# Optimization experiments

Measured on AMD Instinct MI355X. Metric: run time of the kernel, lower is better.

Reference implementation:

```python
import jax, jax.numpy as jnp
import numpy as np

B, T, N = 16, 512, 128
D, HID, S, H, L, EMB = 256, 128, 16, 512, 4, 512
EPS_BN = 1e-5
EPS_LN = 1e-5


def _ln(x, w, b):
    mu = x.mean(-1, keepdims=True)
    v = ((x - mu) ** 2).mean(-1, keepdims=True)
    return (x - mu) * jax.lax.rsqrt(v + EPS_LN) * w + b


def _bn(x, w, b):
    # x: (M, N, C); training-mode BatchNorm1d over (batch, spatial), biased var
    mu = x.mean((0, 1))
    v = x.var((0, 1))
    return (x - mu) * jax.lax.rsqrt(v + EPS_BN) * w + b


def setup_inputs() -> dict:
    key = jax.random.key(0)
    ks = iter(jax.random.split(key, 40))
    r = lambda *s: jax.random.normal(next(ks), s, jnp.float32) * 0.05
    inp = dict(
        x=jax.random.normal(next(ks), (B, T, N, 3), jnp.float32),
        lengths=jax.random.randint(next(ks), (B,), 0, T),
        conv1_w=r(HID, 3), bn1_w=1.0 + r(HID), bn1_b=r(HID),
        conv2_w=r(HID, HID), bn2_w=1.0 + r(HID), bn2_b=r(HID),
        fproj_w=r(D, HID), fproj_b=r(D),
        pre_ln_w=1.0 + r(D), pre_ln_b=r(D),
        in_w=r(L, 2 * H, D), in_b=r(L, 2 * H),
        conv_w=r(L, H, 1, 4), conv_b=r(L, H),
        A=r(L, H, S), Bm=r(L, H, S),
        out_w=r(L, D, H), out_b=r(L, D),
        post_ln_w=1.0 + r(D), post_ln_b=r(D),
        m1_w=r(1024, D), m1_b=r(1024),
        m2_w=r(1024, 1024), m2_b=r(1024),
        m3_w=r(EMB, 1024), m3_b=r(EMB),
    )
    return inp


def reference(x, lengths, conv1_w, bn1_w, bn1_b, conv2_w, bn2_w, bn2_b,
              fproj_w, fproj_b, pre_ln_w, pre_ln_b,
              in_w, in_b, conv_w, conv_b, A, Bm, out_w, out_b,
              post_ln_w, post_ln_b, m1_w, m1_b, m2_w, m2_b, m3_w, m3_b):
    Bb, Tt, Nn, _ = x.shape
    xf = x.reshape(Bb * Tt, Nn, 3)
    mu = xf.mean(1, keepdims=True)
    sd = jnp.std(xf, axis=1, ddof=1, keepdims=True) + 1e-10  # torch.std unbiased
    xn = (xf - mu) / sd

    # PointNet frame encoder (1x1 convs == per-point matmuls)
    h1 = jax.nn.relu(_bn(xn @ conv1_w.T, bn1_w, bn1_b))      # (BT, N, HID)
    h2 = jax.nn.relu(_bn(h1 @ conv2_w.T, bn2_w, bn2_b))
    feat = h2.max(1) @ fproj_w.T + fproj_b                   # (BT, D)

    seq = _ln(feat.reshape(Bb, Tt, D), pre_ln_w, pre_ln_b)
    mask = (jnp.arange(Tt)[None, :] < lengths[:, None]).astype(seq.dtype)  # (B, T)
    mk = mask[:, :, None]

    def mamba(seq, iw, ib, cw, cb, Ai, Bi, ow, ob):
        inp = seq @ iw.T + ib                                # (B, T, 2H)
        Hh = inp.shape[-1] // 2
        gate = jax.nn.sigmoid(inp[..., :Hh])
        upd = jax.nn.silu(inp[..., Hh:])
        u = jax.lax.conv_general_dilated(
            upd.transpose(0, 2, 1), cw, (1,), [(2, 2)],
            feature_group_count=Hh, dimension_numbers=('NCH', 'OIH', 'NCH'))
        u = (u + cb[:, None])[:, :, :seq.shape[1]].transpose(0, 2, 1)  # drop extra step
        # masked linear state scan == masked cumulative sum
        Bu = jnp.einsum('bth,hs->bts', u, Bi) * mk           # (B, T, S)
        hstate = jnp.cumsum(Bu, axis=1)
        out = jnp.einsum('bts,hs->bth', hstate, Ai) * gate * mk
        return out @ ow.T + ob

    for i in range(L):
        seq = mamba(seq, in_w[i], in_b[i], conv_w[i], conv_b[i], A[i], Bm[i], out_w[i], out_b[i])

    seq = _ln(seq, post_ln_w, post_ln_b)
    denom = jnp.maximum(lengths, 1).astype(seq.dtype)[:, None]
    pooled = (seq * mk).sum(1) / denom

    e = jax.nn.gelu(pooled @ m1_w.T + m1_b, approximate=False)
    e = jax.nn.gelu(e @ m2_w.T + m2_b, approximate=False)
    e = e @ m3_w.T + m3_b
    return e / jnp.maximum(jnp.linalg.norm(e, axis=1, keepdims=True), 1e-12)
```

## Files before the change

kernel.cpp:

```cpp
#include <hip/hip_runtime.h>
#include <hip/hip_bf16.h>
#include <math.h>

#define NFRM 8192
#define NPT  128
#define CH   128
#define DD   256
#define HH   512
#define SS   16
#define NL   4

typedef __attribute__((ext_vector_type(8))) short bf16x8;
typedef __attribute__((ext_vector_type(4))) float f32x4;
typedef unsigned short u16;

#define MFMA16 __builtin_amdgcn_mfma_f32_16x16x32_bf16


__device__ __forceinline__ float red256(float v, int tid, volatile float* sc) {
#pragma unroll
  for (int off = 32; off; off >>= 1) v += __shfl_down(v, off);
  __syncthreads();
  if ((tid & 63) == 0) sc[tid >> 6] = v;
  __syncthreads();
  return sc[0] + sc[1] + sc[2] + sc[3];
}

__device__ __forceinline__ float sigmoidf_(float x) { return 1.f / (1.f + __expf(-x)); }
__device__ __forceinline__ float geluf_(float x) { return 0.5f * x * (1.f + erff(x * 0.70710678118654752f)); }

__device__ __forceinline__ u16 f2bf(float f) {
  __hip_bfloat16 h = __float2bfloat16(f);
  return *(u16*)&h;
}
__device__ __forceinline__ float bf2f(u16 u) {
  union { unsigned int i; float f; } v; v.i = ((unsigned int)u) << 16; return v.f;
}


__global__ __launch_bounds__(256) void k_prep(const float* __restrict__ conv2_w,
    const float* __restrict__ fproj_w, const float* __restrict__ in_w, const float* __restrict__ out_w,
    const float* __restrict__ A, const float* __restrict__ Bm,
    const float* __restrict__ cw, const float* __restrict__ cb,
    u16* __restrict__ W2B, u16* __restrict__ fprojB, u16* __restrict__ inwB,
    u16* __restrict__ outwB, u16* __restrict__ albB, u16* __restrict__ BmTd,
    float* __restrict__ cbB) {
  int idx = blockIdx.x * 256 + threadIdx.x;
  if (idx < 16384) {
    int c = idx >> 7, k = idx & 127;
    int dst = c * 128 + ((((k >> 3) ^ (c & 7)) << 3) | (k & 7));
    W2B[dst] = f2bf(conv2_w[idx]);
    return;
  }
  idx -= 16384;
  if (idx < 8192) {
    float4 v = ((const float4*)fproj_w)[idx];
    ushort4 o; o.x = f2bf(v.x); o.y = f2bf(v.y); o.z = f2bf(v.z); o.w = f2bf(v.w);
    ((ushort4*)fprojB)[idx] = o;
    return;
  }
  idx -= 8192;
  if (idx < 262144) {
    float4 v = ((const float4*)in_w)[idx];
    ushort4 o; o.x = f2bf(v.x); o.y = f2bf(v.y); o.z = f2bf(v.z); o.w = f2bf(v.w);
    ((ushort4*)inwB)[idx] = o;
    return;
  }
  idx -= 262144;
  if (idx < 131072) {
    float4 v = ((const float4*)out_w)[idx];
    ushort4 o; o.x = f2bf(v.x); o.y = f2bf(v.y); o.z = f2bf(v.z); o.w = f2bf(v.w);
    ((ushort4*)outwB)[idx] = o;
    return;
  }
  idx -= 131072;
  if (idx < 65536) {
    int l = idx >> 14, rem = idx & 16383, h = rem >> 5, kk = rem & 31;
    albB[idx] = (kk < 16) ? f2bf(A[(size_t)l * 8192 + h * 16 + kk]) : (u16)0;
    return;
  }
  idx -= 65536;
  if (idx < 131072) {
    int l = idx >> 15, rem = idx & 32767;
    int d = rem >> 13, rem2 = rem & 8191, s = rem2 >> 9, h = rem2 & 511;
    BmTd[idx] = f2bf(cw[(size_t)l * 2048 + h * 4 + d] * Bm[(size_t)l * 8192 + h * 16 + s]);
    return;
  }
  idx -= 131072;
  if (idx < 4096) {
    int wsl = idx >> 6, lane = idx & 63;
    int l = wsl >> 4, s = wsl & 15;
    float acc = 0.f;
    for (int h = lane; h < 512; h += 64)
      acc = fmaf(cb[l * 512 + h], Bm[(size_t)l * 8192 + h * 16 + s], acc);
#pragma unroll
    for (int off = 32; off; off >>= 1) acc += __shfl_down(acc, off);
    if (lane == 0) cbB[wsl] = acc;
  }
}

__global__ __launch_bounds__(256) void k_mom(const float* __restrict__ x, float* __restrict__ msd,
                                             float* __restrict__ pstat) {
  __shared__ float mpart[4][6];
  int tid = threadIdx.x, lane = tid & 63, w = tid >> 6;
  int f = blockIdx.x * 4 + w;
  const float* xf = x + (size_t)f * 384 + lane * 6;
  float a0 = xf[0], a1 = xf[1], a2 = xf[2], b0 = xf[3], b1 = xf[4], b2 = xf[5];
  float s0 = a0 + b0, s1 = a1 + b1, s2 = a2 + b2;
  float p00 = a0*a0 + b0*b0, p01 = a0*a1 + b0*b1, p02 = a0*a2 + b0*b2;
  float p11 = a1*a1 + b1*b1, p12 = a1*a2 + b1*b2, p22 = a2*a2 + b2*b2;
#pragma unroll
  for (int off = 32; off; off >>= 1) {
    s0 += __shfl_down(s0, off); s1 += __shfl_down(s1, off); s2 += __shfl_down(s2, off);
    p00 += __shfl_down(p00, off); p01 += __shfl_down(p01, off); p02 += __shfl_down(p02, off);
    p11 += __shfl_down(p11, off); p12 += __shfl_down(p12, off); p22 += __shfl_down(p22, off);
  }
  if (lane == 0) {
    float mu0 = s0 * (1.f/128.f), mu1 = s1 * (1.f/128.f), mu2 = s2 * (1.f/128.f);
    float C00 = p00 - 128.f*mu0*mu0, C01 = p01 - 128.f*mu0*mu1, C02 = p02 - 128.f*mu0*mu2;
    float C11 = p11 - 128.f*mu1*mu1, C12 = p12 - 128.f*mu1*mu2, C22 = p22 - 128.f*mu2*mu2;
    float sd0 = sqrtf(C00 * (1.f/127.f)) + 1e-10f;
    float sd1 = sqrtf(C11 * (1.f/127.f)) + 1e-10f;
    float sd2 = sqrtf(C22 * (1.f/127.f)) + 1e-10f;
    mpart[w][0] = C00/(sd0*sd0); mpart[w][1] = C01/(sd0*sd1); mpart[w][2] = C02/(sd0*sd2);
    mpart[w][3] = C11/(sd1*sd1); mpart[w][4] = C12/(sd1*sd2); mpart[w][5] = C22/(sd2*sd2);
    float* d = msd + (size_t)f * 8;
    d[0] = mu0; d[1] = mu1; d[2] = mu2; d[3] = 0.f;
    d[4] = 1.f/sd0; d[5] = 1.f/sd1; d[6] = 1.f/sd2; d[7] = 0.f;
  }
  __syncthreads();
  if (tid < 8) {
    float tot = 0.f;
    if (tid < 6) { for (int w2 = 0; w2 < 4; ++w2) tot += mpart[w2][tid]; }
    pstat[blockIdx.x * 8 + tid] = tot;
  }
}

__global__ __launch_bounds__(256) void k_stats2(const float* __restrict__ pstat, const float* __restrict__ w1,
    const float* __restrict__ bw, const float* __restrict__ bb, float* __restrict__ cc) {
  __shared__ float part[32][8];
  __shared__ float Mt[8];
  int tid = threadIdx.x, j = tid & 7, g = tid >> 3;
  float sm = 0.f;
  for (int r = g; r < 2048; r += 32) sm += pstat[r * 8 + j];
  part[g][j] = sm;
  __syncthreads();
  if (tid < 8) { float tot = 0.f; for (int g2 = 0; g2 < 32; ++g2) tot += part[g2][tid]; Mt[tid] = tot; }
  __syncthreads();
  if (tid < 128) {
    float w0 = w1[tid*3], wa = w1[tid*3+1], wb = w1[tid*3+2];
    float var = (w0*w0*Mt[0] + wa*wa*Mt[3] + wb*wb*Mt[5]
               + 2.f*(w0*wa*Mt[1] + w0*wb*Mt[2] + wa*wb*Mt[4])) * (1.f/1048576.f);
    float s = bw[tid] / sqrtf(var + 1e-5f);
    ((float4*)cc)[tid] = make_float4(s*w0, s*wa, s*wb, bb[tid]);
  }
}

__global__ __launch_bounds__(256) void k2_main(const float* __restrict__ x, const float4* __restrict__ cc,
    const float4* __restrict__ msd4, const u16* __restrict__ W2B,
    float* __restrict__ z2mx, float* __restrict__ z2mn,
    float* __restrict__ psum, float* __restrict__ psq) {
  __shared__ alignas(16) u16 w2s[16384];
  __shared__ float4 ccs[144];
  __shared__ float smx[2][4][CH], smn[2][4][CH], ssm[2][4][CH], ssq[2][4][CH];
  int tid = threadIdx.x;
  for (int i = tid; i < 2048; i += 256) ((float4*)w2s)[i] = ((const float4*)W2B)[i];
  if (tid < 128) ccs[tid + (tid >> 3)] = cc[tid];
  int lane = tid & 63, w = tid >> 6;
  int lr = lane & 15, kg = lane >> 4;
  int row0 = w * 32 + lr, row1 = row0 + 16;
  int f0i = blockIdx.x * 8;
  float4 mu4 = msd4[f0i * 2], rs4 = msd4[f0i * 2 + 1];
  const float* xr0 = x + (size_t)f0i * 384 + row0 * 3;
  const float* xr1 = x + (size_t)f0i * 384 + row1 * 3;
  float cx0 = xr0[0], cx1 = xr0[1], cx2 = xr0[2];
  float cx3 = xr1[0], cx4 = xr1[1], cx5 = xr1[2];
  __syncthreads();
  for (int fi = 0; fi < 8; ++fi) {
    int f = blockIdx.x * 8 + fi;
    int p = fi & 1;
    float xa0 = (cx0 - mu4.x) * rs4.x, xa1 = (cx1 - mu4.y) * rs4.y, xa2 = (cx2 - mu4.z) * rs4.z;
    float xb0 = (cx3 - mu4.x) * rs4.x, xb1 = (cx4 - mu4.y) * rs4.y, xb2 = (cx5 - mu4.z) * rs4.z;
    int fn = (f + 1 < NFRM) ? f + 1 : f;
    float4 nmu = msd4[fn * 2], nrs = msd4[fn * 2 + 1];
    const float* nr0 = x + (size_t)fn * 384 + row0 * 3;
    const float* nr1 = x + (size_t)fn * 384 + row1 * 3;
    float nx0 = nr0[0], nx1 = nr0[1], nx2 = nr0[2];
    float nx3 = nr1[0], nx4 = nr1[1], nx5 = nr1[2];
    f32x4 acc[2][8];
#pragma unroll
    for (int fr = 0; fr < 2; ++fr)
#pragma unroll
      for (int fc = 0; fc < 8; ++fc) acc[fr][fc] = (f32x4){0.f, 0.f, 0.f, 0.f};
#pragma unroll
    for (int ks = 0; ks < 4; ++ks) {
      int kc = ks * 4 + kg;
      int base9 = kc * 9;
      bf16x8 a0, a1;
#pragma unroll
      for (int q = 0; q < 8; ++q) {
        float4 c4 = ccs[base9 + q];
        float h0 = fmaxf(0.f, fmaf(xa0, c4.x, fmaf(xa1, c4.y, fmaf(xa2, c4.z, c4.w))));
        float h1 = fmaxf(0.f, fmaf(xb0, c4.x, fmaf(xb1, c4.y, fmaf(xb2, c4.z, c4.w))));
        a0[q] = (short)f2bf(h0); a1[q] = (short)f2bf(h1);
      }
#pragma unroll
      for (int fc = 0; fc < 8; ++fc) {
        int col = fc * 16 + lr;
        bf16x8 b = *(const bf16x8*)&w2s[col * 128 + ((kc ^ (col & 7)) << 3)];
        acc[0][fc] = MFMA16(a0, b, acc[0][fc], 0, 0, 0);
        acc[1][fc] = MFMA16(a1, b, acc[1][fc], 0, 0, 0);
      }
    }
#pragma unroll
    for (int fc = 0; fc < 8; ++fc) {
      float mx = -3e38f, mn = 3e38f, sm = 0.f, sq = 0.f;
#pragma unroll
      for (int fr = 0; fr < 2; ++fr)
#pragma unroll
        for (int r = 0; r < 4; ++r) {
          float v = acc[fr][fc][r];
          mx = fmaxf(mx, v); mn = fminf(mn, v); sm += v; sq = fmaf(v, v, sq);
        }
#pragma unroll
      for (int off = 16; off <= 32; off <<= 1) {
        mx = fmaxf(mx, __shfl_xor(mx, off));
        mn = fminf(mn, __shfl_xor(mn, off));
        sm += __shfl_xor(sm, off);
        sq += __shfl_xor(sq, off);
      }
      if (lane < 16) {
        int col = fc * 16 + lr;
        smx[p][w][col] = mx; smn[p][w][col] = mn; ssm[p][w][col] = sm; ssq[p][w][col] = sq;
      }
    }
    __syncthreads();
    if (tid < CH) {
      float mx = smx[p][0][tid], mn = smn[p][0][tid], sm = ssm[p][0][tid], sq = ssq[p][0][tid];
#pragma unroll
      for (int w2 = 1; w2 < 4; ++w2) {
        mx = fmaxf(mx, smx[p][w2][tid]); mn = fminf(mn, smn[p][w2][tid]);
        sm += ssm[p][w2][tid]; sq += ssq[p][w2][tid];
      }
      z2mx[(size_t)f * CH + tid] = mx;
      z2mn[(size_t)f * CH + tid] = mn;
      psum[(size_t)f * CH + tid] = sm;
      psq[(size_t)f * CH + tid]  = sq;
    }
    cx0 = nx0; cx1 = nx1; cx2 = nx2; cx3 = nx3; cx4 = nx4; cx5 = nx5;
    mu4 = nmu; rs4 = nrs;
  }
}

__global__ __launch_bounds__(256) void k_red1(const float* __restrict__ psum, const float* __restrict__ psq,
    float* __restrict__ prs, float* __restrict__ prq) {
  __shared__ float s0[2][128], s1[2][128];
  int tid = threadIdx.x, c = tid & 127, half = tid >> 7;
  int f0 = blockIdx.x * 128;
  float sm = 0.f, sq = 0.f;
  for (int fl = half; fl < 128; fl += 2) {
    size_t idx = (size_t)(f0 + fl) * 128 + c;
    sm += psum[idx]; sq += psq[idx];
  }
  s0[half][c] = sm; s1[half][c] = sq;
  __syncthreads();
  if (tid < 128) {
    prs[blockIdx.x * 128 + tid] = s0[0][tid] + s0[1][tid];
    prq[blockIdx.x * 128 + tid] = s1[0][tid] + s1[1][tid];
  }
}

__global__ __launch_bounds__(256) void k_red2(const float* __restrict__ prs, const float* __restrict__ prq,
    const float* __restrict__ w, const float* __restrict__ b, float* __restrict__ st,
    float invM, float eps) {
  __shared__ float s0[2][128], s1[2][128];
  int tid = threadIdx.x, c = tid & 127, half = tid >> 7;
  float sm = 0.f, sq = 0.f;
  for (int g = half; g < 64; g += 2) { sm += prs[g * 128 + c]; sq += prq[g * 128 + c]; }
  s0[half][c] = sm; s1[half][c] = sq;
  __syncthreads();
  if (tid < 128) {
    float tsm = s0[0][tid] + s0[1][tid], tsq = s1[0][tid] + s1[1][tid];
    float mean = tsm * invM;
    float var = tsq * invM - mean * mean;
    float s = w[tid] / sqrtf(var + eps);
    st[tid] = s;
    st[CH + tid] = b[tid] - mean * s;
  }
}

__global__ __launch_bounds__(512) void k_fi(const float* __restrict__ z2mx, const float* __restrict__ z2mn,
    const float* __restrict__ s2t2, const u16* __restrict__ fprojB, const float* __restrict__ fpb,
    const float* __restrict__ plw, const float* __restrict__ plb,
    const u16* __restrict__ inwB_l, const float* __restrict__ inb,
    u16* __restrict__ gate, u16* __restrict__ upd) {
  __shared__ alignas(16) u16 h2s[32 * 128];
  __shared__ float ft[32 * 260];
  __shared__ alignas(16) u16 as[32 * 256];
  int f0 = blockIdx.x * 32, tid = threadIdx.x;
  int lane = tid & 63, w = tid >> 6, lr = lane & 15, kg = lane >> 4;
  {
    int row = tid >> 4, cc = tid & 15, c0 = cc * 8;
    const float* zx = z2mx + (size_t)(f0 + row) * 128 + c0;
    const float* zn = z2mn + (size_t)(f0 + row) * 128 + c0;
    bf16x8 v;
#pragma unroll
    for (int q = 0; q < 8; ++q) {
      int c = c0 + q;
      float s = s2t2[c], t = s2t2[128 + c];
      float z = (s >= 0.f) ? zx[q] : zn[q];
      v[q] = (short)f2bf(fmaxf(0.f, fmaf(s, z, t)));
    }
    *(bf16x8*)&h2s[row * 128 + ((cc ^ (row & 7)) << 3)] = v;
  }
  __syncthreads();
  {
    f32x4 fac[2][2];
#pragma unroll
    for (int fr = 0; fr < 2; ++fr)
#pragma unroll
      for (int fc = 0; fc < 2; ++fc) fac[fr][fc] = (f32x4){0.f, 0.f, 0.f, 0.f};
#pragma unroll
    for (int ks = 0; ks < 4; ++ks) {
      int kc = ks * 4 + kg;
      bf16x8 a0 = *(const bf16x8*)&h2s[lr * 128 + ((kc ^ (lr & 7)) << 3)];
      bf16x8 a1 = *(const bf16x8*)&h2s[(16 + lr) * 128 + ((kc ^ (lr & 7)) << 3)];
#pragma unroll
      for (int fc = 0; fc < 2; ++fc) {
        int d = w * 32 + fc * 16 + lr;
        bf16x8 b = *(const bf16x8*)&fprojB[(size_t)d * 128 + kc * 8];
        fac[0][fc] = MFMA16(a0, b, fac[0][fc], 0, 0, 0);
        fac[1][fc] = MFMA16(a1, b, fac[1][fc], 0, 0, 0);
      }
    }
#pragma unroll
    for (int fr = 0; fr < 2; ++fr)
#pragma unroll
      for (int fc = 0; fc < 2; ++fc) {
        int d = w * 32 + fc * 16 + lr;
        float bias = fpb[d];
#pragma unroll
        for (int r = 0; r < 4; ++r) {
          int row = fr * 16 + kg * 4 + r;
          ft[row * 260 + d] = fac[fr][fc][r] + bias;
        }
      }
  }
  __syncthreads();
  {
    float4 plw4 = ((const float4*)plw)[lane];
    float4 plb4 = ((const float4*)plb)[lane];
#pragma unroll
    for (int q = 0; q < 4; ++q) {
      int row = w * 4 + q;
      float4 v = *(const float4*)&ft[row * 260 + lane * 4];
      float s = v.x + v.y + v.z + v.w;
#pragma unroll
      for (int off = 32; off; off >>= 1) s += __shfl_xor(s, off);
      float mu = s * (1.f / 256.f);
      float4 dd = make_float4(v.x - mu, v.y - mu, v.z - mu, v.w - mu);
      float qq = dd.x*dd.x + dd.y*dd.y + dd.z*dd.z + dd.w*dd.w;
#pragma unroll
      for (int off = 32; off; off >>= 1) qq += __shfl_xor(qq, off);
      float rs = 1.f / sqrtf(qq * (1.f / 256.f) + 1e-5f);
      u16 o[4];
      o[0] = f2bf(fmaf(dd.x * rs, plw4.x, plb4.x));
      o[1] = f2bf(fmaf(dd.y * rs, plw4.y, plb4.y));
      o[2] = f2bf(fmaf(dd.z * rs, plw4.z, plb4.z));
      o[3] = f2bf(fmaf(dd.w * rs, plw4.w, plb4.w));
      int chunk = lane >> 1;
      *(uint2*)&as[row * 256 + ((chunk ^ (row & 7)) << 3) + (lane & 1) * 4] = *(uint2*)o;
    }
  }
  __syncthreads();
  f32x4 acc[2][8];
#pragma unroll
  for (int fr = 0; fr < 2; ++fr)
#pragma unroll
    for (int fc = 0; fc < 8; ++fc) acc[fr][fc] = (f32x4){0.f, 0.f, 0.f, 0.f};
  int colb = w * 128;
#pragma unroll
  for (int ks = 0; ks < 8; ++ks) {
    int kc = ks * 4 + kg;
    int r1 = 16 + lr;
    bf16x8 a0 = *(const bf16x8*)&as[lr * 256 + ((kc ^ (lr & 7)) << 3)];
    bf16x8 a1 = *(const bf16x8*)&as[r1 * 256 + ((kc ^ (r1 & 7)) << 3)];
#pragma unroll
    for (int fc = 0; fc < 8; ++fc) {
      int col = colb + fc * 16 + lr;
      bf16x8 b = *(const bf16x8*)&inwB_l[(size_t)col * 256 + kc * 8];
      acc[0][fc] = MFMA16(a0, b, acc[0][fc], 0, 0, 0);
      acc[1][fc] = MFMA16(a1, b, acc[1][fc], 0, 0, 0);
    }
  }
  bool isGate = (w < 4);
  u16* dst = isGate ? gate : upd;
  int cbOff = isGate ? 0 : 512;
#pragma unroll
  for (int fr = 0; fr < 2; ++fr)
#pragma unroll
    for (int fc = 0; fc < 8; ++fc) {
      int cg = colb + fc * 16 + lr;
      float bias = inb[cg];
      int colOut = cg - cbOff;
#pragma unroll
      for (int r = 0; r < 4; ++r) {
        int frame = f0 + fr * 16 + kg * 4 + r;
        float v = acc[fr][fc][r] + bias;
        float sg = sigmoidf_(v);
        v = isGate ? sg : v * sg;
        dst[(size_t)frame * 512 + colOut] = f2bf(v);
      }
    }
}

__global__ __launch_bounds__(256) void k_bu(const u16* __restrict__ updB, const u16* __restrict__ BmTd_l,
    const float* __restrict__ cbB_l, const int* __restrict__ lengths, float* __restrict__ bu) {
  __shared__ float part[2][32][16];
  int tid = threadIdx.x, lane = tid & 63, w = tid >> 6;
  int wf = w & 1, hh = w >> 1;
  int f0 = blockIdx.x * 32 + wf * 16;
  int lr = lane & 15, kg = lane >> 4;
  int t = (f0 & 511) + lr;
  const u16* arow = updB + (size_t)(f0 + lr) * 512;
  bool v0 = (t >= 2), v1 = (t >= 1), v3 = (t <= 510);
  const bf16x8 zv = (bf16x8){0,0,0,0,0,0,0,0};
  f32x4 acc = (f32x4){0.f, 0.f, 0.f, 0.f};
#pragma unroll
  for (int ks = 0; ks < 8; ++ks) {
    int kc = hh * 32 + ks * 4 + kg, co = kc * 8;
    bf16x8 a0 = v0 ? *(const bf16x8*)&arow[co - 1024] : zv;
    bf16x8 a1 = v1 ? *(const bf16x8*)&arow[co - 512]  : zv;
    bf16x8 a2 =      *(const bf16x8*)&arow[co];
    bf16x8 a3 = v3 ? *(const bf16x8*)&arow[co + 512]  : zv;
    acc = MFMA16(a0, *(const bf16x8*)&BmTd_l[0 * 8192 + lr * 512 + co], acc, 0, 0, 0);
    acc = MFMA16(a1, *(const bf16x8*)&BmTd_l[1 * 8192 + lr * 512 + co], acc, 0, 0, 0);
    acc = MFMA16(a2, *(const bf16x8*)&BmTd_l[2 * 8192 + lr * 512 + co], acc, 0, 0, 0);
    acc = MFMA16(a3, *(const bf16x8*)&BmTd_l[3 * 8192 + lr * 512 + co], acc, 0, 0, 0);
  }
#pragma unroll
  for (int r = 0; r < 4; ++r) part[hh][wf * 16 + kg * 4 + r][lr] = acc[r];
  __syncthreads();
  int len = lengths[blockIdx.x >> 4];
  for (int i = tid; i < 512; i += 256) {
    int fl = i >> 4, s = i & 15;
    int frame = blockIdx.x * 32 + fl;
    int tt = frame & 511, bi = frame >> 9;
    float val = part[0][fl][s] + part[1][fl][s] + cbB_l[s];
    bu[((size_t)bi * 16 + s) * 512 + tt] = (tt < len) ? val : 0.f;
  }
}

__global__ __launch_bounds__(512) void k_mo(const float* __restrict__ bu,
    u16* __restrict__ gateB, u16* __restrict__ updB,
    const u16* __restrict__ albB_l, const u16* __restrict__ outwB_l, const float* __restrict__ outb,
    const u16* __restrict__ inwB_n, const float* __restrict__ inb_n,
    const int* __restrict__ lengths) {
  __shared__ alignas(16) u16 hsb[32 * 40];
  __shared__ alignas(16) u16 vl[32 * 512];
  __shared__ alignas(16) u16 as[32 * 256];
  int f0 = blockIdx.x * 32, tid = threadIdx.x;
  int bb = f0 >> 9, tbase = f0 & 511;
  int len = lengths[bb];
  int lane = tid & 63, w = tid >> 6, lr = lane & 15, kg = lane >> 4;
  for (int i = tid; i < 640; i += 512) ((unsigned int*)hsb)[i] = 0;
  __syncthreads();
#pragma unroll
  for (int q = 0; q < 2; ++q) {
    int s = w * 2 + q;
    const float* src = bu + ((size_t)bb * 16 + s) * 512 + lane * 8;
    float4 v0 = *(const float4*)src, v1 = *(const float4*)(src + 4);
    float p0 = v0.x, p1 = p0 + v0.y, p2 = p1 + v0.z, p3 = p2 + v0.w;
    float p4 = p3 + v1.x, p5 = p4 + v1.y, p6 = p5 + v1.z, p7 = p6 + v1.w;
    float tot = p7;
#pragma unroll
    for (int off = 1; off < 64; off <<= 1) {
      float n = __shfl_up(tot, off);
      if (lane >= off) tot += n;
    }
    float excl = tot - p7;
    int rbase = lane * 8 - tbase;
    if (rbase >= 0 && rbase < 32) {
      hsb[(rbase + 0) * 40 + s] = f2bf(p0 + excl);
      hsb[(rbase + 1) * 40 + s] = f2bf(p1 + excl);
      hsb[(rbase + 2) * 40 + s] = f2bf(p2 + excl);
      hsb[(rbase + 3) * 40 + s] = f2bf(p3 + excl);
      hsb[(rbase + 4) * 40 + s] = f2bf(p4 + excl);
      hsb[(rbase + 5) * 40 + s] = f2bf(p5 + excl);
      hsb[(rbase + 6) * 40 + s] = f2bf(p6 + excl);
      hsb[(rbase + 7) * 40 + s] = f2bf(p7 + excl);
    }
  }
  __syncthreads();
  {
    bf16x8 a0 = *(const bf16x8*)&hsb[lr * 40 + kg * 8];
    bf16x8 a1 = *(const bf16x8*)&hsb[(16 + lr) * 40 + kg * 8];
    f32x4 zero = (f32x4){0.f, 0.f, 0.f, 0.f};
#pragma unroll
    for (int fc = 0; fc < 4; ++fc) {
      int h = w * 64 + fc * 16 + lr;
      bf16x8 b = *(const bf16x8*)&albB_l[h * 32 + kg * 8];
      f32x4 va = MFMA16(a0, b, zero, 0, 0, 0);
      f32x4 vb = MFMA16(a1, b, zero, 0, 0, 0);
      int hck = h >> 3, hlo = h & 7;
#pragma unroll
      for (int fr = 0; fr < 2; ++fr) {
        f32x4 vv = fr ? vb : va;
#pragma unroll
        for (int r = 0; r < 4; ++r) {
          int fl = fr * 16 + kg * 4 + r;
          int frame = f0 + fl;
          float g = bf2f(gateB[(size_t)frame * 512 + h]);
          float val = ((frame & 511) < len) ? vv[r] * g : 0.f;
          vl[fl * 512 + ((hck ^ (fl & 7)) << 3) + hlo] = f2bf(val);
        }
      }
    }
  }
  __syncthreads();
  {
    f32x4 acc2[2][2];
#pragma unroll
    for (int fr = 0; fr < 2; ++fr)
#pragma unroll
      for (int fc = 0; fc < 2; ++fc) acc2[fr][fc] = (f32x4){0.f, 0.f, 0.f, 0.f};
    int db = w * 32;
#pragma unroll
    for (int ks = 0; ks < 16; ++ks) {
      int kc = ks * 4 + kg;
      int r1 = 16 + lr;
      bf16x8 a0 = *(const bf16x8*)&vl[lr * 512 + ((kc ^ (lr & 7)) << 3)];
      bf16x8 a1 = *(const bf16x8*)&vl[r1 * 512 + ((kc ^ (r1 & 7)) << 3)];
#pragma unroll
      for (int fc = 0; fc < 2; ++fc) {
        int d = db + fc * 16 + lr;
        bf16x8 b = *(const bf16x8*)&outwB_l[(size_t)d * 512 + kc * 8];
        acc2[0][fc] = MFMA16(a0, b, acc2[0][fc], 0, 0, 0);
        acc2[1][fc] = MFMA16(a1, b, acc2[1][fc], 0, 0, 0);
      }
    }
#pragma unroll
    for (int fr = 0; fr < 2; ++fr)
#pragma unroll
      for (int fc = 0; fc < 2; ++fc) {
        int d = db + fc * 16 + lr;
        float bias = outb[d];
        int dck = d >> 3, dlo = d & 7;
#pragma unroll
        for (int r = 0; r < 4; ++r) {
          int row = fr * 16 + kg * 4 + r;
          as[row * 256 + ((dck ^ (row & 7)) << 3) + dlo] = f2bf(acc2[fr][fc][r] + bias);
        }
      }
  }
  __syncthreads();
  f32x4 acc[2][8];
#pragma unroll
  for (int fr = 0; fr < 2; ++fr)
#pragma unroll
    for (int fc = 0; fc < 8; ++fc) acc[fr][fc] = (f32x4){0.f, 0.f, 0.f, 0.f};
  int colb = w * 128;
#pragma unroll
  for (int ks = 0; ks < 8; ++ks) {
    int kc = ks * 4 + kg;
    int r1 = 16 + lr;
    bf16x8 a0 = *(const bf16x8*)&as[lr * 256 + ((kc ^ (lr & 7)) << 3)];
    bf16x8 a1 = *(const bf16x8*)&as[r1 * 256 + ((kc ^ (r1 & 7)) << 3)];
#pragma unroll
    for (int fc = 0; fc < 8; ++fc) {
      int col = colb + fc * 16 + lr;
      bf16x8 b = *(const bf16x8*)&inwB_n[(size_t)col * 256 + kc * 8];
      acc[0][fc] = MFMA16(a0, b, acc[0][fc], 0, 0, 0);
      acc[1][fc] = MFMA16(a1, b, acc[1][fc], 0, 0, 0);
    }
  }
  bool isGate = (w < 4);
  u16* dst = isGate ? gateB : updB;
  int cbOff = isGate ? 0 : 512;
#pragma unroll
  for (int fr = 0; fr < 2; ++fr)
#pragma unroll
    for (int fc = 0; fc < 8; ++fc) {
      int cg = colb + fc * 16 + lr;
      float bias = inb_n[cg];
      int colOut = cg - cbOff;
#pragma unroll
      for (int r = 0; r < 4; ++r) {
        int frame = f0 + fr * 16 + kg * 4 + r;
        float v = acc[fr][fc][r] + bias;
        float sg = sigmoidf_(v);
        v = isGate ? sg : v * sg;
        dst[(size_t)frame * 512 + colOut] = f2bf(v);
      }
    }
}

__global__ __launch_bounds__(256) void k_out(const float* __restrict__ bu, const u16* __restrict__ gateB,
    const u16* __restrict__ albB_l, const u16* __restrict__ outwB_l, const float* __restrict__ outb,
    const int* __restrict__ lengths, float* __restrict__ sout) {
  __shared__ alignas(16) u16 hsb[32 * 40];
  __shared__ alignas(16) u16 vl[32 * 512];
  int f0 = blockIdx.x * 32, tid = threadIdx.x;
  int bb = f0 >> 9, tbase = f0 & 511;
  int len = lengths[bb];
  int lane = tid & 63, w = tid >> 6, lr = lane & 15, kg = lane >> 4;
  for (int i = tid; i < 640; i += 256) ((unsigned int*)hsb)[i] = 0;
  __syncthreads();
#pragma unroll
  for (int q = 0; q < 4; ++q) {
    int s = w * 4 + q;
    const float* src = bu + ((size_t)bb * 16 + s) * 512 + lane * 8;
    float4 v0 = *(const float4*)src, v1 = *(const float4*)(src + 4);
    float p0 = v0.x, p1 = p0 + v0.y, p2 = p1 + v0.z, p3 = p2 + v0.w;
    float p4 = p3 + v1.x, p5 = p4 + v1.y, p6 = p5 + v1.z, p7 = p6 + v1.w;
    float tot = p7;
#pragma unroll
    for (int off = 1; off < 64; off <<= 1) {
      float n = __shfl_up(tot, off);
      if (lane >= off) tot += n;
    }
    float excl = tot - p7;
    int rbase = lane * 8 - tbase;
    if (rbase >= 0 && rbase < 32) {
      hsb[(rbase + 0) * 40 + s] = f2bf(p0 + excl);
      hsb[(rbase + 1) * 40 + s] = f2bf(p1 + excl);
      hsb[(rbase + 2) * 40 + s] = f2bf(p2 + excl);
      hsb[(rbase + 3) * 40 + s] = f2bf(p3 + excl);
      hsb[(rbase + 4) * 40 + s] = f2bf(p4 + excl);
      hsb[(rbase + 5) * 40 + s] = f2bf(p5 + excl);
      hsb[(rbase + 6) * 40 + s] = f2bf(p6 + excl);
      hsb[(rbase + 7) * 40 + s] = f2bf(p7 + excl);
    }
  }
  __syncthreads();
  {
    bf16x8 a0 = *(const bf16x8*)&hsb[lr * 40 + kg * 8];
    bf16x8 a1 = *(const bf16x8*)&hsb[(16 + lr) * 40 + kg * 8];
    f32x4 zero = (f32x4){0.f, 0.f, 0.f, 0.f};
#pragma unroll
    for (int fc = 0; fc < 8; ++fc) {
      int h = w * 128 + fc * 16 + lr;
      bf16x8 b = *(const bf16x8*)&albB_l[h * 32 + kg * 8];
      f32x4 va = MFMA16(a0, b, zero, 0, 0, 0);
      f32x4 vb = MFMA16(a1, b, zero, 0, 0, 0);
      int hck = h >> 3, hlo = h & 7;
#pragma unroll
      for (int fr = 0; fr < 2; ++fr) {
        f32x4 vv = fr ? vb : va;
#pragma unroll
        for (int r = 0; r < 4; ++r) {
          int fl = fr * 16 + kg * 4 + r;
          int frame = f0 + fl;
          float g = bf2f(gateB[(size_t)frame * 512 + h]);
          float val = ((frame & 511) < len) ? vv[r] * g : 0.f;
          vl[fl * 512 + ((hck ^ (fl & 7)) << 3) + hlo] = f2bf(val);
        }
      }
    }
  }
  __syncthreads();
  f32x4 acc[2][4];
#pragma unroll
  for (int fr = 0; fr < 2; ++fr)
#pragma unroll
    for (int fc = 0; fc < 4; ++fc) acc[fr][fc] = (f32x4){0.f, 0.f, 0.f, 0.f};
  int db = w * 64;
#pragma unroll
  for (int ks = 0; ks < 16; ++ks) {
    int kc = ks * 4 + kg;
    int r1 = 16 + lr;
    bf16x8 a0 = *(const bf16x8*)&vl[lr * 512 + ((kc ^ (lr & 7)) << 3)];
    bf16x8 a1 = *(const bf16x8*)&vl[r1 * 512 + ((kc ^ (r1 & 7)) << 3)];
#pragma unroll
    for (int fc = 0; fc < 4; ++fc) {
      int d = db + fc * 16 + lr;
      bf16x8 b = *(const bf16x8*)&outwB_l[(size_t)d * 512 + kc * 8];
      acc[0][fc] = MFMA16(a0, b, acc[0][fc], 0, 0, 0);
      acc[1][fc] = MFMA16(a1, b, acc[1][fc], 0, 0, 0);
    }
  }
#pragma unroll
  for (int fr = 0; fr < 2; ++fr)
#pragma unroll
    for (int fc = 0; fc < 4; ++fc) {
      int d = db + fc * 16 + lr;
      float bias = outb[d];
#pragma unroll
      for (int r = 0; r < 4; ++r) {
        int frame = f0 + fr * 16 + kg * 4 + r;
        sout[(size_t)frame * 256 + d] = acc[fr][fc][r] + bias;
      }
    }
}

__global__ __launch_bounds__(512) void k_pp(const float* __restrict__ seq, const int* __restrict__ lengths,
    const float* __restrict__ w, const float* __restrict__ b, float* __restrict__ pooled) {
  __shared__ float4 part[8][64];
  int bb = blockIdx.x, tid = threadIdx.x, lane = tid & 63, wv = tid >> 6;
  int len = lengths[bb];
  float4 w4 = ((const float4*)w)[lane], b4 = ((const float4*)b)[lane];
  float4 pacc = make_float4(0.f, 0.f, 0.f, 0.f);
  for (int it = 0; it < 64; ++it) {
    int t = it * 8 + wv;
    float4 v = ((const float4*)(seq + ((size_t)bb * 512 + t) * DD))[lane];
    float s = v.x + v.y + v.z + v.w;
#pragma unroll
    for (int off = 32; off; off >>= 1) s += __shfl_xor(s, off);
    float mu = s * (1.f / 256.f);
    float4 dd = make_float4(v.x - mu, v.y - mu, v.z - mu, v.w - mu);
    float q = dd.x*dd.x + dd.y*dd.y + dd.z*dd.z + dd.w*dd.w;
#pragma unroll
    for (int off = 32; off; off >>= 1) q += __shfl_xor(q, off);
    float rs = 1.f / sqrtf(q * (1.f / 256.f) + 1e-5f);
    if (t < len) {
      pacc.x += fmaf(dd.x * rs, w4.x, b4.x);
      pacc.y += fmaf(dd.y * rs, w4.y, b4.y);
      pacc.z += fmaf(dd.z * rs, w4.z, b4.z);
      pacc.w += fmaf(dd.w * rs, w4.w, b4.w);
    }
  }
  part[wv][lane] = pacc;
  __syncthreads();
  if (tid < 64) {
    float4 a = part[0][tid];
#pragma unroll
    for (int w2 = 1; w2 < 8; ++w2) {
      float4 p = part[w2][tid];
      a.x += p.x; a.y += p.y; a.z += p.z; a.w += p.w;
    }
    float inv = 1.f / (float)max(len, 1);
    ((float4*)(pooled + (size_t)bb * DD))[tid] = make_float4(a.x * inv, a.y * inv, a.z * inv, a.w * inv);
  }
}

__global__ __launch_bounds__(256) void k_mlp(const float* __restrict__ in, const float* __restrict__ W,
    const float* __restrict__ bias, float* __restrict__ out, int K, int Nout, int act) {
  __shared__ float lin[16 * 1024];
  int tid = threadIdx.x, lane = tid & 63, w = tid >> 6;
  for (int i = tid; i < 16 * K / 4; i += 256) ((float4*)lin)[i] = ((const float4*)in)[i];
  __syncthreads();
  int o = blockIdx.x * 4 + w;
  const float4* wr4 = (const float4*)(W + (size_t)o * K);
  float acc[16];
#pragma unroll
  for (int r = 0; r < 16; ++r) acc[r] = 0.f;
  for (int k4 = lane; k4 < K / 4; k4 += 64) {
    float4 wv = wr4[k4];
    int kb = k4 * 4;
#pragma unroll
    for (int r = 0; r < 16; ++r) {
      float4 lv = *(const float4*)&lin[r * K + kb];
      acc[r] = fmaf(lv.x, wv.x, fmaf(lv.y, wv.y, fmaf(lv.z, wv.z, fmaf(lv.w, wv.w, acc[r]))));
    }
  }
#pragma unroll
  for (int r = 0; r < 16; ++r) {
#pragma unroll
    for (int off = 32; off; off >>= 1) acc[r] += __shfl_xor(acc[r], off);
  }
  if (lane < 16) {
    float v = 0.f;
#pragma unroll
    for (int r = 0; r < 16; ++r) if (lane == r) v = acc[r];
    v += bias[o];
    if (act) v = geluf_(v);
    out[(size_t)lane * Nout + o] = v;
  }
}

__global__ __launch_bounds__(256) void k_norm(const float* __restrict__ e, float* __restrict__ out) {
  __shared__ float sc[4];
  int b = blockIdx.x, tid = threadIdx.x;
  float v0 = e[(size_t)b * 512 + tid], v1 = e[(size_t)b * 512 + 256 + tid];
  float ss = red256(v0 * v0 + v1 * v1, tid, sc);
  float nrm = fmaxf(sqrtf(ss), 1e-12f);
  out[(size_t)b * 512 + tid] = v0 / nrm;
  out[(size_t)b * 512 + 256 + tid] = v1 / nrm;
}


extern "C" void kernel_launch(void* const* d_in, const int* in_sizes, int n_in,
                              void* d_out, int out_size, void* d_ws, size_t ws_size,
                              hipStream_t stream) {
  const float* x         = (const float*)d_in[0];
  const int*   lengths   = (const int*)d_in[1];
  const float* conv1_w   = (const float*)d_in[2];
  const float* bn1_w     = (const float*)d_in[3];
  const float* bn1_b     = (const float*)d_in[4];
  const float* conv2_w   = (const float*)d_in[5];
  const float* bn2_w     = (const float*)d_in[6];
  const float* bn2_b     = (const float*)d_in[7];
  const float* fproj_w   = (const float*)d_in[8];
  const float* fproj_b   = (const float*)d_in[9];
  const float* pre_ln_w  = (const float*)d_in[10];
  const float* pre_ln_b  = (const float*)d_in[11];
  const float* in_w      = (const float*)d_in[12];
  const float* in_b      = (const float*)d_in[13];
  const float* conv_w    = (const float*)d_in[14];
  const float* conv_b    = (const float*)d_in[15];
  const float* A         = (const float*)d_in[16];
  const float* Bm        = (const float*)d_in[17];
  const float* out_w     = (const float*)d_in[18];
  const float* out_b     = (const float*)d_in[19];
  const float* post_ln_w = (const float*)d_in[20];
  const float* post_ln_b = (const float*)d_in[21];
  const float* m1_w      = (const float*)d_in[22];
  const float* m1_b      = (const float*)d_in[23];
  const float* m2_w      = (const float*)d_in[24];
  const float* m2_b      = (const float*)d_in[25];
  const float* m3_w      = (const float*)d_in[26];
  const float* m3_b      = (const float*)d_in[27];
  float* outp = (float*)d_out;

  float* wsf = (float*)d_ws;
  size_t o = 0;
  auto F32 = [&](size_t n) { float* p = wsf + o; o += (n + 63) & ~(size_t)63; return p; };
  float* psum   = F32(1048576);
  float* psq    = F32(1048576);
  float* z2mx   = F32(1048576);
  float* z2mn   = F32(1048576);
  float* msd    = F32(65536);
  float* pstat  = F32(16384);
  float* cc     = F32(512);
  float* s2t2   = F32(256);
  float* prs    = F32(8192);
  float* prq    = F32(8192);
  u16*   W2B    = (u16*)F32(8192);
  u16*   fprojB = (u16*)F32(16384);
  u16*   inwB   = (u16*)F32(524288);
  u16*   outwB  = (u16*)F32(262144);
  u16*   albB   = (u16*)F32(32768);
  u16*   BmTd   = (u16*)F32(65536);
  float* cbB    = F32(64);
  float* seqA   = F32(2097152);
  u16*   gateB  = (u16*)F32(2097152);
  u16*   updB   = (u16*)F32(2097152);
  float* buv    = F32(131072);
  float* pooled = F32(4096);
  float* e1     = F32(16384);
  float* e2     = F32(16384);
  float* e3     = F32(8192);
  if (ws_size < o * sizeof(float)) return;

  const float invM = 1.f / (float)(NFRM * NPT);

  k_prep<<<2416, 256, 0, stream>>>(conv2_w, fproj_w, in_w, out_w, A, Bm, conv_w, conv_b,
                                   W2B, fprojB, inwB, outwB, albB, BmTd, cbB);
  k_mom<<<2048, 256, 0, stream>>>(x, msd, pstat);
  k_stats2<<<1, 256, 0, stream>>>(pstat, conv1_w, bn1_w, bn1_b, cc);
  k2_main<<<NFRM / 8, 256, 0, stream>>>(x, (const float4*)cc, (const float4*)msd, W2B,
                                        z2mx, z2mn, psum, psq);
  k_red1<<<64, 256, 0, stream>>>(psum, psq, prs, prq);
  k_red2<<<1, 256, 0, stream>>>(prs, prq, bn2_w, bn2_b, s2t2, invM, 1e-5f);
  k_fi<<<NFRM / 32, 512, 0, stream>>>(z2mx, z2mn, s2t2, fprojB, fproj_b, pre_ln_w, pre_ln_b,
                                      inwB, in_b, gateB, updB);

  for (int l = 0; l < 3; ++l) {
    k_bu<<<NFRM / 32, 256, 0, stream>>>(updB, BmTd + (size_t)l * 32768, cbB + l * 16, lengths, buv);
    k_mo<<<NFRM / 32, 512, 0, stream>>>(buv, gateB, updB,
                                        albB + (size_t)l * 16384, outwB + (size_t)l * 131072,
                                        out_b + l * 256,
                                        inwB + (size_t)(l + 1) * 262144, in_b + (l + 1) * 1024,
                                        lengths);
  }
  k_bu<<<NFRM / 32, 256, 0, stream>>>(updB, BmTd + (size_t)3 * 32768, cbB + 3 * 16, lengths, buv);
  k_out<<<NFRM / 32, 256, 0, stream>>>(buv, gateB, albB + (size_t)3 * 16384,
                                       outwB + (size_t)3 * 131072, out_b + 3 * 256, lengths, seqA);
  k_pp<<<16, 512, 0, stream>>>(seqA, lengths, post_ln_w, post_ln_b, pooled);
  k_mlp<<<256, 256, 0, stream>>>(pooled, m1_w, m1_b, e1, 256, 1024, 1);
  k_mlp<<<256, 256, 0, stream>>>(e1, m2_w, m2_b, e2, 1024, 1024, 1);
  k_mlp<<<128, 256, 0, stream>>>(e2, m3_w, m3_b, e3, 1024, 512, 0);
  k_norm<<<16, 256, 0, stream>>>(e3, outp);
}
```

Baseline: 406.4 us.

## Write per-wave partial stats directly and defer cross-wave reduction to consumers

k2_main no longer combines the four waves' max/min/sum/sumsq through shared memory with a per-frame __syncthreads. Each wave writes its own partials to global buffers that are four times larger, and k_red1 and k_fi fold the extra wave dimension when they read. The block also handles 4 frames instead of 8, which doubles the grid. This removes a barrier and shared-memory round trip per frame, at the cost of roughly 4x more global writes and reads for the intermediate stats and more reloading of the W2 weights into LDS per block.

```diff
diff --git a/kernel.cpp b/kernel.cpp
--- a/kernel.cpp
+++ b/kernel.cpp
@@ -158,27 +158,25 @@
 
 __global__ __launch_bounds__(256) void k2_main(const float* __restrict__ x, const float4* __restrict__ cc,
     const float4* __restrict__ msd4, const u16* __restrict__ W2B,
-    float* __restrict__ z2mx, float* __restrict__ z2mn,
-    float* __restrict__ psum, float* __restrict__ psq) {
+    float* __restrict__ z2mxP, float* __restrict__ z2mnP,
+    float* __restrict__ psumP, float* __restrict__ psqP) {
   __shared__ alignas(16) u16 w2s[16384];
   __shared__ float4 ccs[144];
-  __shared__ float smx[2][4][CH], smn[2][4][CH], ssm[2][4][CH], ssq[2][4][CH];
   int tid = threadIdx.x;
   for (int i = tid; i < 2048; i += 256) ((float4*)w2s)[i] = ((const float4*)W2B)[i];
   if (tid < 128) ccs[tid + (tid >> 3)] = cc[tid];
   int lane = tid & 63, w = tid >> 6;
   int lr = lane & 15, kg = lane >> 4;
   int row0 = w * 32 + lr, row1 = row0 + 16;
-  int f0i = blockIdx.x * 8;
+  int f0i = blockIdx.x * 4;
   float4 mu4 = msd4[f0i * 2], rs4 = msd4[f0i * 2 + 1];
   const float* xr0 = x + (size_t)f0i * 384 + row0 * 3;
   const float* xr1 = x + (size_t)f0i * 384 + row1 * 3;
   float cx0 = xr0[0], cx1 = xr0[1], cx2 = xr0[2];
   float cx3 = xr1[0], cx4 = xr1[1], cx5 = xr1[2];
   __syncthreads();
-  for (int fi = 0; fi < 8; ++fi) {
-    int f = blockIdx.x * 8 + fi;
-    int p = fi & 1;
+  for (int fi = 0; fi < 4; ++fi) {
+    int f = blockIdx.x * 4 + fi;
     float xa0 = (cx0 - mu4.x) * rs4.x, xa1 = (cx1 - mu4.y) * rs4.y, xa2 = (cx2 - mu4.z) * rs4.z;
     float xb0 = (cx3 - mu4.x) * rs4.x, xb1 = (cx4 - mu4.y) * rs4.y, xb2 = (cx5 - mu4.z) * rs4.z;
     int fn = (f + 1 < NFRM) ? f + 1 : f;
@@ -212,6 +210,7 @@
         acc[1][fc] = MFMA16(a1, b, acc[1][fc], 0, 0, 0);
       }
     }
+    size_t pbase = ((size_t)f * 4 + w) * 128;
 #pragma unroll
     for (int fc = 0; fc < 8; ++fc) {
       float mx = -3e38f, mn = 3e38f, sm = 0.f, sq = 0.f;
@@ -230,37 +229,24 @@
         sq += __shfl_xor(sq, off);
       }
       if (lane < 16) {
-        int col = fc * 16 + lr;
-        smx[p][w][col] = mx; smn[p][w][col] = mn; ssm[p][w][col] = sm; ssq[p][w][col] = sq;
-      }
-    }
-    __syncthreads();
-    if (tid < CH) {
-      float mx = smx[p][0][tid], mn = smn[p][0][tid], sm = ssm[p][0][tid], sq = ssq[p][0][tid];
-#pragma unroll
-      for (int w2 = 1; w2 < 4; ++w2) {
-        mx = fmaxf(mx, smx[p][w2][tid]); mn = fminf(mn, smn[p][w2][tid]);
-        sm += ssm[p][w2][tid]; sq += ssq[p][w2][tid];
-      }
-      z2mx[(size_t)f * CH + tid] = mx;
-      z2mn[(size_t)f * CH + tid] = mn;
-      psum[(size_t)f * CH + tid] = sm;
-      psq[(size_t)f * CH + tid]  = sq;
+        size_t idx = pbase + fc * 16 + lr;
+        z2mxP[idx] = mx; z2mnP[idx] = mn; psumP[idx] = sm; psqP[idx] = sq;
+      }
     }
     cx0 = nx0; cx1 = nx1; cx2 = nx2; cx3 = nx3; cx4 = nx4; cx5 = nx5;
     mu4 = nmu; rs4 = nrs;
   }
 }
 
-__global__ __launch_bounds__(256) void k_red1(const float* __restrict__ psum, const float* __restrict__ psq,
+__global__ __launch_bounds__(256) void k_red1(const float* __restrict__ psumP, const float* __restrict__ psqP,
     float* __restrict__ prs, float* __restrict__ prq) {
   __shared__ float s0[2][128], s1[2][128];
   int tid = threadIdx.x, c = tid & 127, half = tid >> 7;
-  int f0 = blockIdx.x * 128;
+  int r0 = blockIdx.x * 512;
   float sm = 0.f, sq = 0.f;
-  for (int fl = half; fl < 128; fl += 2) {
-    size_t idx = (size_t)(f0 + fl) * 128 + c;
-    sm += psum[idx]; sq += psq[idx];
+  for (int r = half; r < 512; r += 2) {
+    size_t idx = (size_t)(r0 + r) * 128 + c;
+    sm += psumP[idx]; sq += psqP[idx];
   }
   s0[half][c] = sm; s1[half][c] = sq;
   __syncthreads();
@@ -289,7 +275,7 @@
   }
 }
 
-__global__ __launch_bounds__(512) void k_fi(const float* __restrict__ z2mx, const float* __restrict__ z2mn,
+__global__ __launch_bounds__(512) void k_fi(const float* __restrict__ z2mxP, const float* __restrict__ z2mnP,
     const float* __restrict__ s2t2, const u16* __restrict__ fprojB, const float* __restrict__ fpb,
     const float* __restrict__ plw, const float* __restrict__ plb,
     const u16* __restrict__ inwB_l, const float* __restrict__ inb,
@@ -301,8 +287,20 @@
   int lane = tid & 63, w = tid >> 6, lr = lane & 15, kg = lane >> 4;
   {
     int row = tid >> 4, cc = tid & 15, c0 = cc * 8;
-    const float* zx = z2mx + (size_t)(f0 + row) * 128 + c0;
-    const float* zn = z2mn + (size_t)(f0 + row) * 128 + c0;
+    size_t base = (size_t)(f0 + row) * 512 + c0;
+    float4 xa = *(const float4*)(z2mxP + base),       xb = *(const float4*)(z2mxP + base + 4);
+    float4 na = *(const float4*)(z2mnP + base),       nb = *(const float4*)(z2mnP + base + 4);
+#pragma unroll
+    for (int p = 1; p < 4; ++p) {
+      float4 ya = *(const float4*)(z2mxP + base + p * 128), yb = *(const float4*)(z2mxP + base + p * 128 + 4);
+      float4 ma = *(const float4*)(z2mnP + base + p * 128), mb = *(const float4*)(z2mnP + base + p * 128 + 4);
+      xa.x = fmaxf(xa.x, ya.x); xa.y = fmaxf(xa.y, ya.y); xa.z = fmaxf(xa.z, ya.z); xa.w = fmaxf(xa.w, ya.w);
+      xb.x = fmaxf(xb.x, yb.x); xb.y = fmaxf(xb.y, yb.y); xb.z = fmaxf(xb.z, yb.z); xb.w = fmaxf(xb.w, yb.w);
+      na.x = fminf(na.x, ma.x); na.y = fminf(na.y, ma.y); na.z = fminf(na.z, ma.z); na.w = fminf(na.w, ma.w);
+      nb.x = fminf(nb.x, mb.x); nb.y = fminf(nb.y, mb.y); nb.z = fminf(nb.z, mb.z); nb.w = fminf(nb.w, mb.w);
+    }
+    float zx[8] = {xa.x, xa.y, xa.z, xa.w, xb.x, xb.y, xb.z, xb.w};
+    float zn[8] = {na.x, na.y, na.z, na.w, nb.x, nb.y, nb.z, nb.w};
     bf16x8 v;
 #pragma unroll
     for (int q = 0; q < 8; ++q) {
@@ -815,10 +813,10 @@
   float* wsf = (float*)d_ws;
   size_t o = 0;
   auto F32 = [&](size_t n) { float* p = wsf + o; o += (n + 63) & ~(size_t)63; return p; };
-  float* psum   = F32(1048576);
-  float* psq    = F32(1048576);
-  float* z2mx   = F32(1048576);
-  float* z2mn   = F32(1048576);
+  float* psumP  = F32(4194304);
+  float* psqP   = F32(4194304);
+  float* z2mxP  = F32(4194304);
+  float* z2mnP  = F32(4194304);
   float* msd    = F32(65536);
   float* pstat  = F32(16384);
   float* cc     = F32(512);
@@ -848,11 +846,11 @@
                                    W2B, fprojB, inwB, outwB, albB, BmTd, cbB);
   k_mom<<<2048, 256, 0, stream>>>(x, msd, pstat);
   k_stats2<<<1, 256, 0, stream>>>(pstat, conv1_w, bn1_w, bn1_b, cc);
-  k2_main<<<NFRM / 8, 256, 0, stream>>>(x, (const float4*)cc, (const float4*)msd, W2B,
-                                        z2mx, z2mn, psum, psq);
-  k_red1<<<64, 256, 0, stream>>>(psum, psq, prs, prq);
+  k2_main<<<NFRM / 4, 256, 0, stream>>>(x, (const float4*)cc, (const float4*)msd, W2B,
+                                        z2mxP, z2mnP, psumP, psqP);
+  k_red1<<<64, 256, 0, stream>>>(psumP, psqP, prs, prq);
   k_red2<<<1, 256, 0, stream>>>(prs, prq, bn2_w, bn2_b, s2t2, invM, 1e-5f);
-  k_fi<<<NFRM / 32, 512, 0, stream>>>(z2mx, z2mn, s2t2, fprojB, fproj_b, pre_ln_w, pre_ln_b,
+  k_fi<<<NFRM / 32, 512, 0, stream>>>(z2mxP, z2mnP, s2t2, fprojB, fproj_b, pre_ln_w, pre_ln_b,
                                       inwB, in_b, gateB, updB);
 
   for (int l = 0; l < 3; ++l) {
```

New measurement: 489.6 us. 1.2x slower.
